# Performance work log

Hardware: AMD Instinct MI355X
Metric: run time of the kernel (lower is better)

## Reference

```python
import jax, jax.numpy as jnp
import numpy as np

B, N, D_IN, D_OUT = 512, 64, 2048, 1024
EPS = 1e-12  # layer_norm_epsilon


def setup_inputs() -> dict:
    key = jax.random.key(0)
    k0, k1, k2, k3, k4 = jax.random.split(key, 5)
    img_feats = jax.random.normal(k0, (B, N, D_IN), jnp.float32)
    boxes = jax.random.normal(k1, (B, N, 7), jnp.float32)
    box_mask = jax.random.randint(k2, (B, N), 0, 2, jnp.int32)
    obj_labels = jax.random.randint(k3, (B, N), 0, 91, jnp.int32)
    # Learned params: obj_downsample Linear(2048->1024), LayerNorm(1024)
    W = jax.random.normal(k4, (D_IN, D_OUT), jnp.float32) * 0.02
    b = jnp.zeros((D_OUT,), jnp.float32)
    ln_w = jnp.ones((D_OUT,), jnp.float32)
    ln_b = jnp.zeros((D_OUT,), jnp.float32)
    return {"img_feats": img_feats, "boxes": boxes, "box_mask": box_mask,
            "obj_labels": obj_labels, "W": W, "b": b, "ln_w": ln_w, "ln_b": ln_b}


def reference(img_feats, boxes, box_mask, obj_labels, W, b, ln_w, ln_b):
    # Dropout(p=0.1) is identity in eval mode.
    # Linear + ReLU applied to every (padded) box; per-row ops so padded rows
    # are computed then masked — same math as gathering valid rows first.
    h = jax.nn.relu(jnp.einsum('bnd,df->bnf', img_feats, W) + b)  # [B,N,1024]
    mu = jnp.mean(h, axis=-1, keepdims=True)
    var = jnp.mean(jnp.square(h - mu), axis=-1, keepdims=True)
    ln = (h - mu) * jax.lax.rsqrt(var + EPS) * ln_w + ln_b  # LayerNorm
    # pad_sequence repack: left-align each image's valid boxes (stable sort
    # keeps original order among valid boxes), zero the padded tail.
    order = jnp.argsort(1 - box_mask, axis=1, stable=True)  # valid first
    packed = jnp.take_along_axis(ln, order[:, :, None], axis=1)
    m = jnp.take_along_axis(box_mask, order, axis=1).astype(ln.dtype)
    return packed * m[:, :, None]  # obj_reps: [B, N, 1024]
```

## Files before the change

kernel.cpp:

```cpp
#include <hip/hip_runtime.h>
#include <hip/hip_bf16.h>

typedef __attribute__((ext_vector_type(8))) short short8;
typedef __attribute__((ext_vector_type(4))) short short4v;
typedef __attribute__((ext_vector_type(4))) float f32x4;

#define B_SZ   512
#define N_BOX  64
#define D_IN   2048
#define D_OUT  1024
#define M_ROWS (B_SZ * N_BOX)

__device__ __forceinline__ short f2bf(float x) {
    union { __hip_bfloat16 h; short s; } u;
    u.h = __float2bfloat16(x);
    return u.s;
}
__device__ __forceinline__ float bf2f(short s) {
    union { short s; __hip_bfloat16 h; } u;
    u.s = s;
    return __bfloat162float(u.h);
}

__global__ void cast_a_kernel(const float* __restrict__ in,
                              short* __restrict__ out, int n8) {
    int i = blockIdx.x * blockDim.x + threadIdx.x;
    int stride = gridDim.x * blockDim.x;
    for (int j = i; j < n8; j += stride) {
        long e = (long)j * 8;
        float4 v0 = *(const float4*)(in + e);
        float4 v1 = *(const float4*)(in + e + 4);
        short8 o;
        o[0] = f2bf(v0.x); o[1] = f2bf(v0.y); o[2] = f2bf(v0.z); o[3] = f2bf(v0.w);
        o[4] = f2bf(v1.x); o[5] = f2bf(v1.y); o[6] = f2bf(v1.z); o[7] = f2bf(v1.w);
        *(short8*)(out + e) = o;
    }
}

__global__ void transpose_w_kernel(const float* __restrict__ W,
                                   short* __restrict__ Bt) {
    __shared__ float tile[32][33];
    int c0 = blockIdx.x * 32;
    int r0 = blockIdx.y * 32;
    int tc = threadIdx.x & 31;
    int tr = threadIdx.x >> 5;
#pragma unroll
    for (int i = 0; i < 32; i += 8)
        tile[tr + i][tc] = W[(long)(r0 + tr + i) * D_OUT + c0 + tc];
    __syncthreads();
#pragma unroll
    for (int i = 0; i < 32; i += 8)
        Bt[(long)(c0 + tr + i) * D_IN + r0 + tc] = f2bf(tile[tc][tr + i]);
}

#define HALF_SHORTS 8192


__device__ __forceinline__ void stage_half(const short* __restrict__ mat, long row0, int k0,
                                           short* lds, int tid) {
#pragma unroll
    for (int j = 0; j < 2; ++j) {
        int d = j * 8192 + tid * 16;
        int s = d ^ (((d >> 7) & 7) << 4);
        int row = s >> 7;
        int ke  = (s & 127) >> 1;
        __builtin_amdgcn_global_load_lds(
            (const __attribute__((address_space(1))) void*)(mat + (row0 + row) * D_IN + k0 + ke),
            (__attribute__((address_space(3))) void*)((char*)lds + d), 16, 0, 0);
    }
}

__device__ __forceinline__ short8 ld_frag(const short* lds, int rowh, int kb) {
    int d = (rowh * 128 + kb) ^ ((rowh & 7) << 4);
    return *(const short8*)((const char*)lds + d);
}

#define BAR()   __builtin_amdgcn_s_barrier()
#define LGKM0() do { asm volatile("s_waitcnt lgkmcnt(0)" ::: "memory"); \
                     __builtin_amdgcn_sched_barrier(0); } while (0)
#define VM6()   do { asm volatile("s_waitcnt vmcnt(6)" ::: "memory");  \
                     __builtin_amdgcn_sched_barrier(0); } while (0)

__global__ __launch_bounds__(512, 2)
void gemm256_kernel(const short* __restrict__ A, const short* __restrict__ Bt,
                    const float* __restrict__ bias, short* __restrict__ H) {
    __shared__ short As[4 * HALF_SHORTS];
    __shared__ short Bs[4 * HALF_SHORTS];

    int bid = blockIdx.x;
    int lid = (bid & 7) * 64 + (bid >> 3);
    int bn = lid & 3;
    int bm = lid >> 2;

    int tid  = threadIdx.x;
    int lane = tid & 63;
    int wave = tid >> 6;
    int wm = wave >> 2;
    int wn = wave & 3;
    int bh = wn >> 1;
    int lrow = lane & 15;
    int lkb  = (lane >> 4) * 16;

    const long arow0 = (long)bm * 256;
    const long brow0 = (long)bn * 256;

    f32x4 acc[8][4];
#pragma unroll
    for (int i = 0; i < 8; ++i)
#pragma unroll
        for (int j = 0; j < 4; ++j) acc[i][j] = (f32x4)0.0f;

    const int nt = D_IN / 64;

    stage_half(Bt, brow0,       0,  Bs + 0 * HALF_SHORTS, tid);
    stage_half(Bt, brow0 + 128, 0,  Bs + 1 * HALF_SHORTS, tid);
    stage_half(A,  arow0,       0,  As + 0 * HALF_SHORTS, tid);
    stage_half(A,  arow0 + 128, 0,  As + 1 * HALF_SHORTS, tid);
    stage_half(Bt, brow0,       64, Bs + 2 * HALF_SHORTS, tid);
    stage_half(Bt, brow0 + 128, 64, Bs + 3 * HALF_SHORTS, tid);
    stage_half(A,  arow0,       64, As + 2 * HALF_SHORTS, tid);
    VM6();
    BAR();

    short8 a[2][4], b[2][4];

#pragma unroll 1
    for (int t = 0; t < nt; ++t) {
        int buf  = t & 1;
        int nbuf = buf ^ 1;
        const short* Ah = As + (buf * 2 + wm) * HALF_SHORTS;
        const short* Bh = Bs + (buf * 2 + bh) * HALF_SHORTS;
        short* As_buf = As + buf * 2 * HALF_SHORTS;
        short* Bs_buf = Bs + buf * 2 * HALF_SHORTS;
        int k1 = ((t + 1) & (nt - 1)) * 64;
        int k2 = ((t + 2) & (nt - 1)) * 64;

#pragma unroll
        for (int ks = 0; ks < 2; ++ks) {
#pragma unroll
            for (int mi = 0; mi < 4; ++mi)
                a[ks][mi] = ld_frag(Ah, mi * 16 + lrow, ks * 64 + lkb);
#pragma unroll
            for (int nj = 0; nj < 4; ++nj)
                b[ks][nj] = ld_frag(Bh, (wn & 1) * 64 + nj * 16 + lrow, ks * 64 + lkb);
        }
        stage_half(A, arow0 + 128, k1, As + (nbuf * 2 + 1) * HALF_SHORTS, tid);
        BAR();
        LGKM0();
        __builtin_amdgcn_s_setprio(1);
#pragma unroll
        for (int mi = 0; mi < 4; ++mi)
#pragma unroll
            for (int nj = 0; nj < 2; ++nj)
#pragma unroll
                for (int ks = 0; ks < 2; ++ks)
                    acc[mi][nj] = __builtin_amdgcn_mfma_f32_16x16x32_bf16(
                        a[ks][mi], b[ks][nj], acc[mi][nj], 0, 0, 0);
        __builtin_amdgcn_s_setprio(0);
        BAR();

        stage_half(Bt, brow0, k2, Bs_buf + 0 * HALF_SHORTS, tid);
        BAR();
        __builtin_amdgcn_s_setprio(1);
#pragma unroll
        for (int mi = 0; mi < 4; ++mi)
#pragma unroll
            for (int nj = 2; nj < 4; ++nj)
#pragma unroll
                for (int ks = 0; ks < 2; ++ks)
                    acc[mi][nj] = __builtin_amdgcn_mfma_f32_16x16x32_bf16(
                        a[ks][mi], b[ks][nj], acc[mi][nj], 0, 0, 0);
        __builtin_amdgcn_s_setprio(0);
        BAR();

#pragma unroll
        for (int ks = 0; ks < 2; ++ks)
#pragma unroll
            for (int mi = 0; mi < 4; ++mi)
                a[ks][mi] = ld_frag(Ah, 64 + mi * 16 + lrow, ks * 64 + lkb);
        stage_half(Bt, brow0 + 128, k2, Bs_buf + 1 * HALF_SHORTS, tid);
        BAR();
        LGKM0();
        __builtin_amdgcn_s_setprio(1);
#pragma unroll
        for (int mi = 0; mi < 4; ++mi)
#pragma unroll
            for (int nj = 0; nj < 2; ++nj)
#pragma unroll
                for (int ks = 0; ks < 2; ++ks)
                    acc[4 + mi][nj] = __builtin_amdgcn_mfma_f32_16x16x32_bf16(
                        a[ks][mi], b[ks][nj], acc[4 + mi][nj], 0, 0, 0);
        __builtin_amdgcn_s_setprio(0);
        BAR();

        stage_half(A, arow0, k2, As_buf + 0 * HALF_SHORTS, tid);
        BAR();
        __builtin_amdgcn_s_setprio(1);
#pragma unroll
        for (int mi = 0; mi < 4; ++mi)
#pragma unroll
            for (int nj = 2; nj < 4; ++nj)
#pragma unroll
                for (int ks = 0; ks < 2; ++ks)
                    acc[4 + mi][nj] = __builtin_amdgcn_mfma_f32_16x16x32_bf16(
                        a[ks][mi], b[ks][nj], acc[4 + mi][nj], 0, 0, 0);
        __builtin_amdgcn_s_setprio(0);
        VM6();
        BAR();
    }

    float bb[4];
#pragma unroll
    for (int nj = 0; nj < 4; ++nj)
        bb[nj] = bias[bn * 256 + wn * 64 + nj * 16 + lrow];
#pragma unroll
    for (int mi = 0; mi < 8; ++mi) {
        long row = arow0 + wm * 128 + mi * 16 + (lane >> 4) * 4;
#pragma unroll
        for (int nj = 0; nj < 4; ++nj) {
            int col = bn * 256 + wn * 64 + nj * 16 + lrow;
#pragma unroll
            for (int r = 0; r < 4; ++r) {
                float v = fmaxf(acc[mi][nj][r] + bb[nj], 0.0f);
                H[(row + r) * D_OUT + col] = f2bf(v);
            }
        }
    }
}

__global__ void ln_pack_kernel(const short* __restrict__ H,
                               const int* __restrict__ mask,
                               const float* __restrict__ ln_w,
                               const float* __restrict__ ln_b,
                               float* __restrict__ out) {
    int drow = blockIdx.x;
    int b = drow >> 6, j = drow & 63;
    int tid = threadIdx.x;
    int lane = tid & 63;
    int wave = tid >> 6;
    int base = tid * 4;

    int mv = mask[(b << 6) | lane];
    unsigned long long bal = __ballot(mv != 0);
    int cnt = __popcll(bal);

    float4 o = make_float4(0.f, 0.f, 0.f, 0.f);
    if (j < cnt) {
        int pre = __popcll(bal & ((1ull << lane) - 1ull));
        unsigned long long sel = __ballot(mv != 0 && pre == j);
        int srcn = (int)__builtin_ctzll(sel);
        long row = (long)((b << 6) | srcn);

        short4v hv = *(const short4v*)(H + row * D_OUT + base);
        float v0 = bf2f(hv[0]), v1 = bf2f(hv[1]), v2 = bf2f(hv[2]), v3 = bf2f(hv[3]);

        float s  = v0 + v1 + v2 + v3;
        float s2 = v0 * v0 + v1 * v1 + v2 * v2 + v3 * v3;
#pragma unroll
        for (int off = 32; off > 0; off >>= 1) {
            s  += __shfl_xor(s, off);
            s2 += __shfl_xor(s2, off);
        }
        __shared__ float red[8];
        if (lane == 0) { red[wave] = s; red[wave + 4] = s2; }
        __syncthreads();
        float S  = red[0] + red[1] + red[2] + red[3];
        float S2 = red[4] + red[5] + red[6] + red[7];
        float mu   = S * (1.0f / D_OUT);
        float var  = S2 * (1.0f / D_OUT) - mu * mu;
        float rstd = rsqrtf(var + 1e-12f);

        float4 wv = *(const float4*)(ln_w + base);
        float4 bv = *(const float4*)(ln_b + base);
        o.x = (v0 - mu) * rstd * wv.x + bv.x;
        o.y = (v1 - mu) * rstd * wv.y + bv.y;
        o.z = (v2 - mu) * rstd * wv.z + bv.z;
        o.w = (v3 - mu) * rstd * wv.w + bv.w;
    }
    *(float4*)(out + (long)drow * D_OUT + base) = o;
}

extern "C" void kernel_launch(void* const* d_in, const int* in_sizes, int n_in,
                              void* d_out, int out_size, void* d_ws, size_t ws_size,
                              hipStream_t stream) {
    const float* img  = (const float*)d_in[0];
    const int*   mask = (const int*)d_in[2];
    const float* W    = (const float*)d_in[4];
    const float* bias = (const float*)d_in[5];
    const float* lnw  = (const float*)d_in[6];
    const float* lnb  = (const float*)d_in[7];
    float* out = (float*)d_out;

    short* Abf = (short*)d_out;
    short* Bt  = (short*)d_ws;
    short* H   = (short*)d_ws + (long)D_OUT * D_IN;

    cast_a_kernel<<<2048, 256, 0, stream>>>(img, Abf, M_ROWS * D_IN / 8);
    transpose_w_kernel<<<dim3(D_OUT / 32, D_IN / 32), 256, 0, stream>>>(W, Bt);
    gemm256_kernel<<<(M_ROWS / 256) * (D_OUT / 256), 512, 0, stream>>>(Abf, Bt, bias, H);
    ln_pack_kernel<<<M_ROWS, 256, 0, stream>>>(H, mask, lnw, lnb, out);
}
```

Baseline: 263.3 us.

## Software-pipeline LDS fragment reads across GEMM phases with partial lgkmcnt waits

```diff
diff --git a/kernel.cpp b/kernel.cpp
--- a/kernel.cpp
+++ b/kernel.cpp
@@ -53,11 +53,10 @@
         Bt[(long)(c0 + tr + i) * D_IN + r0 + tc] = f2bf(tile[tc][tr + i]);
 }
 
-#define HALF_SHORTS 8192
-
+#define HALF_BYTES 16384
 
 __device__ __forceinline__ void stage_half(const short* __restrict__ mat, long row0, int k0,
-                                           short* lds, int tid) {
+                                           char* ldsbase, int tid) {
 #pragma unroll
     for (int j = 0; j < 2; ++j) {
         int d = j * 8192 + tid * 16;
@@ -66,26 +65,19 @@
         int ke  = (s & 127) >> 1;
         __builtin_amdgcn_global_load_lds(
             (const __attribute__((address_space(1))) void*)(mat + (row0 + row) * D_IN + k0 + ke),
-            (__attribute__((address_space(3))) void*)((char*)lds + d), 16, 0, 0);
-    }
-}
-
-__device__ __forceinline__ short8 ld_frag(const short* lds, int rowh, int kb) {
-    int d = (rowh * 128 + kb) ^ ((rowh & 7) << 4);
-    return *(const short8*)((const char*)lds + d);
-}
-
-#define BAR()   __builtin_amdgcn_s_barrier()
-#define LGKM0() do { asm volatile("s_waitcnt lgkmcnt(0)" ::: "memory"); \
-                     __builtin_amdgcn_sched_barrier(0); } while (0)
-#define VM6()   do { asm volatile("s_waitcnt vmcnt(6)" ::: "memory");  \
-                     __builtin_amdgcn_sched_barrier(0); } while (0)
+            (__attribute__((address_space(3))) void*)(ldsbase + d), 16, 0, 0);
+    }
+}
+
+#define BAR()    __builtin_amdgcn_s_barrier()
+#define SB0()    __builtin_amdgcn_sched_barrier(0)
+#define LGKM(n)  do { asm volatile("s_waitcnt lgkmcnt(" #n ")" ::: "memory"); SB0(); } while (0)
+#define VMW(n)   do { asm volatile("s_waitcnt vmcnt(" #n ")" ::: "memory"); SB0(); } while (0)
 
 __global__ __launch_bounds__(512, 2)
 void gemm256_kernel(const short* __restrict__ A, const short* __restrict__ Bt,
                     const float* __restrict__ bias, short* __restrict__ H) {
-    __shared__ short As[4 * HALF_SHORTS];
-    __shared__ short Bs[4 * HALF_SHORTS];
+    __shared__ char LDS[131072];
 
     int bid = blockIdx.x;
     int lid = (bid & 7) * 64 + (bid >> 3);
@@ -101,6 +93,14 @@
     int lrow = lane & 15;
     int lkb  = (lane >> 4) * 16;
 
+    int swz = (lrow & 7) << 4;
+    int la0 = (lrow * 128 + lkb) ^ swz;
+    int la1 = (lrow * 128 + 64 + lkb) ^ swz;
+    int aO0 = wm * HALF_BYTES + la0;
+    int aO1 = wm * HALF_BYTES + la1;
+    int bO0 = 65536 + bh * HALF_BYTES + (wn & 1) * 8192 + la0;
+    int bO1 = 65536 + bh * HALF_BYTES + (wn & 1) * 8192 + la1;
+
     const long arow0 = (long)bm * 256;
     const long brow0 = (long)bn * 256;
 
@@ -112,41 +112,38 @@
 
     const int nt = D_IN / 64;
 
-    stage_half(Bt, brow0,       0,  Bs + 0 * HALF_SHORTS, tid);
-    stage_half(Bt, brow0 + 128, 0,  Bs + 1 * HALF_SHORTS, tid);
-    stage_half(A,  arow0,       0,  As + 0 * HALF_SHORTS, tid);
-    stage_half(A,  arow0 + 128, 0,  As + 1 * HALF_SHORTS, tid);
-    stage_half(Bt, brow0,       64, Bs + 2 * HALF_SHORTS, tid);
-    stage_half(Bt, brow0 + 128, 64, Bs + 3 * HALF_SHORTS, tid);
-    stage_half(A,  arow0,       64, As + 2 * HALF_SHORTS, tid);
-    VM6();
-    BAR();
-
-    short8 a[2][4], b[2][4];
+#define RD(off) (*(const short8*)(LDS + (off)))
+
+    stage_half(Bt, brow0,       0,  LDS + 65536,                 tid);
+    stage_half(Bt, brow0 + 128, 0,  LDS + 65536 + HALF_BYTES,    tid);
+    stage_half(A,  arow0,       0,  LDS,                         tid);
+    stage_half(A,  arow0 + 128, 0,  LDS + HALF_BYTES,            tid);
+    stage_half(Bt, brow0,       64, LDS + 65536 + 32768,             tid);
+    stage_half(Bt, brow0 + 128, 64, LDS + 65536 + 32768 + HALF_BYTES, tid);
+    stage_half(A,  arow0,       64, LDS + 32768,                 tid);
+    VMW(6);
+    BAR(); SB0();
+
+    short8 aC[2][4], aN[2][4], bN0[2][2], bN1[2][2];
+#pragma unroll
+    for (int mi = 0; mi < 4; ++mi) { aC[0][mi] = RD(aO0 + mi * 2048); aC[1][mi] = RD(aO1 + mi * 2048); }
+#pragma unroll
+    for (int j = 0; j < 2; ++j)    { bN0[0][j] = RD(bO0 + j * 2048); bN0[1][j] = RD(bO1 + j * 2048); }
 
 #pragma unroll 1
     for (int t = 0; t < nt; ++t) {
-        int buf  = t & 1;
-        int nbuf = buf ^ 1;
-        const short* Ah = As + (buf * 2 + wm) * HALF_SHORTS;
-        const short* Bh = Bs + (buf * 2 + bh) * HALF_SHORTS;
-        short* As_buf = As + buf * 2 * HALF_SHORTS;
-        short* Bs_buf = Bs + buf * 2 * HALF_SHORTS;
+        int bufo  = (t & 1) * 32768;
+        int nbufo = bufo ^ 32768;
         int k1 = ((t + 1) & (nt - 1)) * 64;
         int k2 = ((t + 2) & (nt - 1)) * 64;
 
 #pragma unroll
-        for (int ks = 0; ks < 2; ++ks) {
-#pragma unroll
-            for (int mi = 0; mi < 4; ++mi)
-                a[ks][mi] = ld_frag(Ah, mi * 16 + lrow, ks * 64 + lkb);
-#pragma unroll
-            for (int nj = 0; nj < 4; ++nj)
-                b[ks][nj] = ld_frag(Bh, (wn & 1) * 64 + nj * 16 + lrow, ks * 64 + lkb);
-        }
-        stage_half(A, arow0 + 128, k1, As + (nbuf * 2 + 1) * HALF_SHORTS, tid);
-        BAR();
-        LGKM0();
+        for (int j = 0; j < 2; ++j) {
+            bN1[0][j] = RD(bufo + bO0 + (2 + j) * 2048);
+            bN1[1][j] = RD(bufo + bO1 + (2 + j) * 2048);
+        }
+        stage_half(A, arow0 + 128, k1, LDS + nbufo + HALF_BYTES, tid);
+        LGKM(4);
         __builtin_amdgcn_s_setprio(1);
 #pragma unroll
         for (int mi = 0; mi < 4; ++mi)
@@ -155,32 +152,31 @@
 #pragma unroll
                 for (int ks = 0; ks < 2; ++ks)
                     acc[mi][nj] = __builtin_amdgcn_mfma_f32_16x16x32_bf16(
-                        a[ks][mi], b[ks][nj], acc[mi][nj], 0, 0, 0);
+                        aC[ks][mi], bN0[ks][nj], acc[mi][nj], 0, 0, 0);
         __builtin_amdgcn_s_setprio(0);
-        BAR();
-
-        stage_half(Bt, brow0, k2, Bs_buf + 0 * HALF_SHORTS, tid);
-        BAR();
+
+        BAR(); SB0();
+#pragma unroll
+        for (int mi = 0; mi < 4; ++mi) {
+            aN[0][mi] = RD(bufo + aO0 + 8192 + mi * 2048);
+            aN[1][mi] = RD(bufo + aO1 + 8192 + mi * 2048);
+        }
+        stage_half(Bt, brow0, k2, LDS + 65536 + bufo, tid);
+        LGKM(8);
         __builtin_amdgcn_s_setprio(1);
 #pragma unroll
         for (int mi = 0; mi < 4; ++mi)
 #pragma unroll
-            for (int nj = 2; nj < 4; ++nj)
+            for (int nj = 0; nj < 2; ++nj)
 #pragma unroll
                 for (int ks = 0; ks < 2; ++ks)
-                    acc[mi][nj] = __builtin_amdgcn_mfma_f32_16x16x32_bf16(
-                        a[ks][mi], b[ks][nj], acc[mi][nj], 0, 0, 0);
+                    acc[mi][2 + nj] = __builtin_amdgcn_mfma_f32_16x16x32_bf16(
+                        aC[ks][mi], bN1[ks][nj], acc[mi][2 + nj], 0, 0, 0);
         __builtin_amdgcn_s_setprio(0);
-        BAR();
-
-#pragma unroll
-        for (int ks = 0; ks < 2; ++ks)
-#pragma unroll
-            for (int mi = 0; mi < 4; ++mi)
-                a[ks][mi] = ld_frag(Ah, 64 + mi * 16 + lrow, ks * 64 + lkb);
-        stage_half(Bt, brow0 + 128, k2, Bs_buf + 1 * HALF_SHORTS, tid);
-        BAR();
-        LGKM0();
+
+        BAR(); SB0();
+        stage_half(Bt, brow0 + 128, k2, LDS + 65536 + bufo + HALF_BYTES, tid);
+        LGKM(0);
         __builtin_amdgcn_s_setprio(1);
 #pragma unroll
         for (int mi = 0; mi < 4; ++mi)
@@ -189,25 +185,34 @@
 #pragma unroll
                 for (int ks = 0; ks < 2; ++ks)
                     acc[4 + mi][nj] = __builtin_amdgcn_mfma_f32_16x16x32_bf16(
-                        a[ks][mi], b[ks][nj], acc[4 + mi][nj], 0, 0, 0);
+                        aN[ks][mi], bN0[ks][nj], acc[4 + mi][nj], 0, 0, 0);
         __builtin_amdgcn_s_setprio(0);
-        BAR();
-
-        stage_half(A, arow0, k2, As_buf + 0 * HALF_SHORTS, tid);
-        BAR();
+
+        VMW(4);
+        BAR(); SB0();
+        stage_half(A, arow0, k2, LDS + bufo, tid);
+#pragma unroll
+        for (int mi = 0; mi < 4; ++mi) {
+            aC[0][mi] = RD(nbufo + aO0 + mi * 2048);
+            aC[1][mi] = RD(nbufo + aO1 + mi * 2048);
+        }
+#pragma unroll
+        for (int j = 0; j < 2; ++j) {
+            bN0[0][j] = RD(nbufo + bO0 + j * 2048);
+            bN0[1][j] = RD(nbufo + bO1 + j * 2048);
+        }
         __builtin_amdgcn_s_setprio(1);
 #pragma unroll
         for (int mi = 0; mi < 4; ++mi)
 #pragma unroll
-            for (int nj = 2; nj < 4; ++nj)
+            for (int nj = 0; nj < 2; ++nj)
 #pragma unroll
                 for (int ks = 0; ks < 2; ++ks)
-                    acc[4 + mi][nj] = __builtin_amdgcn_mfma_f32_16x16x32_bf16(
-                        a[ks][mi], b[ks][nj], acc[4 + mi][nj], 0, 0, 0);
+                    acc[4 + mi][2 + nj] = __builtin_amdgcn_mfma_f32_16x16x32_bf16(
+                        aN[ks][mi], bN1[ks][nj], acc[4 + mi][2 + nj], 0, 0, 0);
         __builtin_amdgcn_s_setprio(0);
-        VM6();
-        BAR();
-    }
+    }
+#undef RD
 
     float bb[4];
 #pragma unroll
```

After: 228.9 us. 1.15x faster.
